# Kernel optimization log

Measured on AMD Instinct MI355X. Metric: run time of the kernel, lower is better.

The kernel has to match this reference:

```python
import jax, jax.numpy as jnp
import numpy as np

# NF4 codebook (bitsandbytes normal-float-4 quantiles)
NF4 = jnp.array([-1.0, -0.6961928009986877, -0.5250730514526367, -0.39491748809814453,
                 -0.28444138169288635, -0.18477343022823334, -0.09105003625154495, 0.0,
                 0.07958029955625534, 0.16093020141124725, 0.24611230194568634, 0.33791524171829224,
                 0.44070982933044434, 0.5626170039176941, 0.7229568362236023, 1.0], dtype=jnp.float32)

BLOCK = 64           # bitsandbytes quant blocksize
OUT, IN, R = 4096, 4096, 16
SCALING = 32.0 / 16.0  # lora_alpha / r


def setup_inputs() -> dict:
    key = jax.random.key(0)
    k1, k2, k3, k4 = jax.random.split(key, 4)
    x = jax.random.normal(k1, (4096, IN), dtype=jnp.float32)
    codes = jax.random.randint(k2, (OUT, IN), 0, 16, dtype=jnp.int32)
    scales = jax.random.uniform(k3, (OUT * IN // BLOCK,), dtype=jnp.float32) * 0.1
    lora_A = jax.random.normal(k4, (R, IN), dtype=jnp.float32) * (1.0 / np.sqrt(IN))
    lora_B = jax.random.normal(jax.random.fold_in(key, 7), (OUT, R), dtype=jnp.float32) * 0.02
    return {"x": x, "codes": codes, "scales": scales, "lora_A": lora_A, "lora_B": lora_B}


def dequantize_nf4(codes, scales):
    # codes: [OUT, IN] int in [0,16); scales: one absmax scale per BLOCK contiguous elements
    w = NF4[codes].reshape(-1, BLOCK) * scales[:, None]
    return w.reshape(OUT, IN)  # [out, in]


def reference(x, codes, scales, lora_A, lora_B):
    # Base quantized linear: dequantize then y = x @ W^T  (nn.Linear semantics)
    W = dequantize_nf4(codes, scales)               # [out, in]
    result = x @ W.T                                # [tokens, out]
    # LoRA low-rank correction (dropout p=0.0 -> identity)
    result = result + (x @ lora_A.T) @ lora_B.T * SCALING
    return result
```

## Files before the change

kernel.cpp:

```cpp
#include <hip/hip_runtime.h>
#include <hip/hip_bf16.h>

#define TOKENS 4096
#define OUTN   4096
#define INK    4096
#define RANK   16
#define KP     4160

typedef __attribute__((ext_vector_type(8))) short short8;
typedef __attribute__((ext_vector_type(4))) float f32x4;

__device__ __constant__ float NF4_TAB[16] = {
  -1.0f, -0.6961928009986877f, -0.5250730514526367f, -0.39491748809814453f,
  -0.28444138169288635f, -0.18477343022823334f, -0.09105003625154495f, 0.0f,
  0.07958029955625534f, 0.16093020141124725f, 0.24611230194568634f, 0.33791524171829224f,
  0.44070982933044434f, 0.5626170039176941f, 0.7229568362236023f, 1.0f };

__device__ __forceinline__ unsigned short f2bf(float f) {
  unsigned int u = __float_as_uint(f);
  u += 0x7FFFu + ((u >> 16) & 1u);
  return (unsigned short)(u >> 16);
}

__global__ __launch_bounds__(256) void prep_x_kernel(const float* __restrict__ x,
                                                     const float* __restrict__ loraA,
                                                     unsigned short* __restrict__ Xbf) {
  const int r0 = blockIdx.x * 4;
  const int t = threadIdx.x;
  const int lane = t & 63;
  const int wave = t >> 6;

  float xv[4][16];
  #pragma unroll
  for (int rv = 0; rv < 4; ++rv) {
    const float* xrow = x + (size_t)(r0 + rv) * INK;
    unsigned short* brow = Xbf + (size_t)(r0 + rv) * KP;
    #pragma unroll
    for (int q = 0; q < 4; ++q) {
      const int e0 = q * 1024 + t * 4;
      float4 v = *(const float4*)(xrow + e0);
      xv[rv][q * 4 + 0] = v.x; xv[rv][q * 4 + 1] = v.y;
      xv[rv][q * 4 + 2] = v.z; xv[rv][q * 4 + 3] = v.w;
      ushort4 o; o.x = f2bf(v.x); o.y = f2bf(v.y); o.z = f2bf(v.z); o.w = f2bf(v.w);
      *(ushort4*)(brow + e0) = o;
    }
  }

  float p[4][16];
  #pragma unroll
  for (int a = 0; a < 4; ++a)
    #pragma unroll
    for (int b = 0; b < 16; ++b) p[a][b] = 0.f;

  #pragma unroll
  for (int rr = 0; rr < 16; ++rr) {
    const float* arow = loraA + (size_t)rr * INK;
    float av[16];
    #pragma unroll
    for (int q = 0; q < 4; ++q) {
      float4 v = *(const float4*)(arow + q * 1024 + t * 4);
      av[q * 4 + 0] = v.x; av[q * 4 + 1] = v.y;
      av[q * 4 + 2] = v.z; av[q * 4 + 3] = v.w;
    }
    #pragma unroll
    for (int rv = 0; rv < 4; ++rv) {
      float s = 0.f;
      #pragma unroll
      for (int j = 0; j < 16; ++j) s += xv[rv][j] * av[j];
      p[rv][rr] += s;
    }
  }

  #pragma unroll
  for (int rv = 0; rv < 4; ++rv)
    #pragma unroll
    for (int rr = 0; rr < 16; ++rr) {
      float v = p[rv][rr];
      v += __shfl_xor(v, 32); v += __shfl_xor(v, 16); v += __shfl_xor(v, 8);
      v += __shfl_xor(v, 4);  v += __shfl_xor(v, 2);  v += __shfl_xor(v, 1);
      p[rv][rr] = v;
    }
  __shared__ float red[4][64];
  if (lane == 0) {
    #pragma unroll
    for (int rv = 0; rv < 4; ++rv)
      #pragma unroll
      for (int rr = 0; rr < 16; ++rr) red[wave][rv * 16 + rr] = p[rv][rr];
  }
  __syncthreads();
  if (t < 64) {
    float s = red[0][t] + red[1][t] + red[2][t] + red[3][t];
    int rv = t >> 4, rr = t & 15;
    Xbf[(size_t)(r0 + rv) * KP + INK + rr] = f2bf(s);
  }
}

__global__ __launch_bounds__(256) void prep_w_kernel(const int* __restrict__ codes,
                                                     const float* __restrict__ scales,
                                                     const float* __restrict__ loraB,
                                                     unsigned short* __restrict__ Wbf) {
  __shared__ float tab[16];
  int t = threadIdx.x;
  if (t < 16) tab[t] = NF4_TAB[t];
  __syncthreads();
  const int row = blockIdx.x;
  const int* crow = codes + (size_t)row * INK;
  const float* srow = scales + (row << 6);
  unsigned short* wrow = Wbf + (size_t)row * KP;
  #pragma unroll
  for (int q = 0; q < 4; ++q) {
    const int e0 = q * 1024 + t * 4;
    int4 c = *(const int4*)(crow + e0);
    float sc = srow[e0 >> 6];
    ushort4 o;
    o.x = f2bf(tab[c.x] * sc);
    o.y = f2bf(tab[c.y] * sc);
    o.z = f2bf(tab[c.z] * sc);
    o.w = f2bf(tab[c.w] * sc);
    *(ushort4*)(wrow + e0) = o;
  }
  if (t < RANK) {
    wrow[INK + t] = f2bf(2.0f * loraB[row * RANK + t]);
  } else if (t < 64) {
    wrow[4112 + (t - 16)] = 0;
  }
}

__global__ __launch_bounds__(256, 2) void gemm_kernel(const unsigned short* __restrict__ Xbf,
                                                      const unsigned short* __restrict__ Wbf,
                                                      float* __restrict__ out) {
  __shared__ char lds[32768];
  char* ldsA = lds;
  char* ldsB = lds + 16384;
  const int tid  = threadIdx.x;
  const int lane = tid & 63;
  const int wave = tid >> 6;
  const int wr = wave >> 1, wc = wave & 1;
  const size_t brow = (size_t)blockIdx.y * 128;
  const size_t bcol = (size_t)blockIdx.x * 128;

  f32x4 acc[4][4];
  #pragma unroll
  for (int m = 0; m < 4; ++m)
    #pragma unroll
    for (int n = 0; n < 4; ++n) acc[m][n] = (f32x4){0.f, 0.f, 0.f, 0.f};

  const char* gA[4]; const char* gB[4]; int ldst[4];
  #pragma unroll
  for (int j = 0; j < 4; ++j) {
    int c = (wave * 4 + j) * 64 + lane;
    int r = c >> 3;
    int gkc = (c & 7) ^ (r & 7);
    gA[j] = (const char*)Xbf + ((brow + r) * KP) * 2 + gkc * 16;
    gB[j] = (const char*)Wbf + ((bcol + r) * KP) * 2 + gkc * 16;
    ldst[j] = (wave * 4 + j) * 1024;
  }

  for (int kt = 0; kt < KP / 64; ++kt) {
    const int koff = kt * 128;
    #pragma unroll
    for (int j = 0; j < 4; ++j) {
      __builtin_amdgcn_global_load_lds(
          (const __attribute__((address_space(1))) void*)(gA[j] + koff),
          (__attribute__((address_space(3))) void*)(ldsA + ldst[j]), 16, 0, 0);
      __builtin_amdgcn_global_load_lds(
          (const __attribute__((address_space(1))) void*)(gB[j] + koff),
          (__attribute__((address_space(3))) void*)(ldsB + ldst[j]), 16, 0, 0);
    }
    __syncthreads();

    short8 af[4][2], bfr[4][2];
    #pragma unroll
    for (int m = 0; m < 4; ++m) {
      int r  = wr * 64 + m * 16 + (lane & 15);
      int x0 = (lane >> 4) * 16;
      int sw = (r & 7) << 4;
      af[m][0] = *(const short8*)(ldsA + r * 128 + ((x0) ^ sw));
      af[m][1] = *(const short8*)(ldsA + r * 128 + ((64 + x0) ^ sw));
    }
    #pragma unroll
    for (int n = 0; n < 4; ++n) {
      int r  = wc * 64 + n * 16 + (lane & 15);
      int x0 = (lane >> 4) * 16;
      int sw = (r & 7) << 4;
      bfr[n][0] = *(const short8*)(ldsB + r * 128 + ((x0) ^ sw));
      bfr[n][1] = *(const short8*)(ldsB + r * 128 + ((64 + x0) ^ sw));
    }
    #pragma unroll
    for (int s = 0; s < 2; ++s)
      #pragma unroll
      for (int m = 0; m < 4; ++m)
        #pragma unroll
        for (int n = 0; n < 4; ++n)
          acc[m][n] = __builtin_amdgcn_mfma_f32_16x16x32_bf16(af[m][s], bfr[n][s], acc[m][n], 0, 0, 0);
    __syncthreads();
  }

  #pragma unroll
  for (int m = 0; m < 4; ++m) {
    int row = (int)brow + wr * 64 + m * 16 + ((lane >> 4) << 2);
    #pragma unroll
    for (int n = 0; n < 4; ++n) {
      int col = (int)bcol + wc * 64 + n * 16 + (lane & 15);
      #pragma unroll
      for (int j = 0; j < 4; ++j)
        out[(size_t)(row + j) * OUTN + col] = acc[m][n][j];
    }
  }
}

extern "C" void kernel_launch(void* const* d_in, const int* in_sizes, int n_in,
                              void* d_out, int out_size, void* d_ws, size_t ws_size,
                              hipStream_t stream) {
  const float* x      = (const float*)d_in[0];
  const int*   codes  = (const int*)d_in[1];
  const float* scales = (const float*)d_in[2];
  const float* loraA  = (const float*)d_in[3];
  const float* loraB  = (const float*)d_in[4];
  float* out = (float*)d_out;

  unsigned short* Xbf = (unsigned short*)d_ws;
  unsigned short* Wbf = Xbf + (size_t)TOKENS * KP;

  prep_x_kernel<<<TOKENS / 4, 256, 0, stream>>>(x, loraA, Xbf);
  prep_w_kernel<<<OUTN, 256, 0, stream>>>(codes, scales, loraB, Wbf);

  dim3 grid(OUTN / 128, TOKENS / 128);
  gemm_kernel<<<grid, 256, 0, stream>>>(Xbf, Wbf, out);
}
```

Baseline: 325.2 us.

## Restructure GEMM into 256x256 tiles with double-buffered LDS and interleaved MFMA/load phases

The GEMM moves from 128x128 tiles with 4 waves and a single LDS buffer to 256x256 tiles with 8 waves and 128KB of dynamic LDS split into two buffers. Global-to-LDS loads for the next k-steps are issued in quarter-phases between four MFMA sub-blocks, with explicit vmcnt waits, barriers and setprio. The goal is to hide load latency behind compute and raise arithmetic intensity per byte loaded. In exchange it needs more registers and LDS, cuts occupancy, and launches only 256 blocks, which may leave some CUs idle.

```diff
diff --git a/kernel.cpp b/kernel.cpp
--- a/kernel.cpp
+++ b/kernel.cpp
@@ -6,6 +6,7 @@
 #define INK    4096
 #define RANK   16
 #define KP     4160
+#define NT     (KP/64)
 
 typedef __attribute__((ext_vector_type(8))) short short8;
 typedef __attribute__((ext_vector_type(4))) float f32x4;
@@ -126,82 +127,174 @@
   }
 }
 
-__global__ __launch_bounds__(256, 2) void gemm_kernel(const unsigned short* __restrict__ Xbf,
+#define STAGE2(BASE, OFFS, LDSB, BUF, H, KT)                                               \
+  do {                                                                                     \
+    __builtin_amdgcn_global_load_lds(                                                      \
+        (const __attribute__((address_space(1))) void*)((BASE) + (OFFS)[H][0] + (KT)*128), \
+        (__attribute__((address_space(3))) void*)((LDSB) + (BUF)*32768 + (H)*16384 + tid*16), 16, 0, 0); \
+    __builtin_amdgcn_global_load_lds(                                                      \
+        (const __attribute__((address_space(1))) void*)((BASE) + (OFFS)[H][1] + (KT)*128), \
+        (__attribute__((address_space(3))) void*)((LDSB) + (BUF)*32768 + (H)*16384 + 8192 + tid*16), 16, 0, 0); \
+  } while (0)
+
+__global__ __launch_bounds__(512, 2) void gemm_kernel(const unsigned short* __restrict__ Xbf,
                                                       const unsigned short* __restrict__ Wbf,
                                                       float* __restrict__ out) {
-  __shared__ char lds[32768];
+  extern __shared__ char lds[];
   char* ldsA = lds;
-  char* ldsB = lds + 16384;
+  char* ldsB = lds + 65536;
   const int tid  = threadIdx.x;
   const int lane = tid & 63;
   const int wave = tid >> 6;
-  const int wr = wave >> 1, wc = wave & 1;
-  const size_t brow = (size_t)blockIdx.y * 128;
-  const size_t bcol = (size_t)blockIdx.x * 128;
-
-  f32x4 acc[4][4];
-  #pragma unroll
-  for (int m = 0; m < 4; ++m)
+  const int wr = wave >> 2;
+  const int wc = wave & 3;
+  const int brow = blockIdx.y * 256;
+  const int bcol = blockIdx.x * 256;
+
+  unsigned int aoffg[2][2], boffg[2][2];
+  #pragma unroll
+  for (int h = 0; h < 2; ++h)
+    #pragma unroll
+    for (int j = 0; j < 2; ++j) {
+      int ci  = j * 512 + tid;
+      int lr  = ci >> 3;
+      int gkc = (ci & 7) ^ (lr & 7);
+      int growA = (lr & 63) | (h << 6) | ((lr >> 6) << 7);
+      int growB = (lr & 31) | (h << 5) | ((lr >> 5) << 6);
+      aoffg[h][j] = (unsigned)growA * (KP * 2) + gkc * 16;
+      boffg[h][j] = (unsigned)growB * (KP * 2) + gkc * 16;
+    }
+  const char* baseA = (const char*)Xbf + (size_t)brow * (KP * 2);
+  const char* baseB = (const char*)Wbf + (size_t)bcol * (KP * 2);
+
+  unsigned int aoff[8][2], boff[4][2];
+  #pragma unroll
+  for (int m = 0; m < 8; ++m) {
+    int R = wr * 128 + m * 16 + (lane & 15);
+    int h = (R >> 6) & 1;
+    int lr = (R & 63) | ((R >> 7) << 6);
+    #pragma unroll
+    for (int s = 0; s < 2; ++s) {
+      int c = s * 4 + (lane >> 4);
+      aoff[m][s] = h * 16384 + lr * 128 + ((c ^ (lr & 7)) * 16);
+    }
+  }
+  #pragma unroll
+  for (int n = 0; n < 4; ++n) {
+    int C = wc * 64 + n * 16 + (lane & 15);
+    int h = (C >> 5) & 1;
+    int lc = (C & 31) | ((C >> 6) << 5);
+    #pragma unroll
+    for (int s = 0; s < 2; ++s) {
+      int c = s * 4 + (lane >> 4);
+      boff[n][s] = h * 16384 + lc * 128 + ((c ^ (lc & 7)) * 16);
+    }
+  }
+
+  f32x4 acc[8][4];
+  #pragma unroll
+  for (int m = 0; m < 8; ++m)
     #pragma unroll
     for (int n = 0; n < 4; ++n) acc[m][n] = (f32x4){0.f, 0.f, 0.f, 0.f};
 
-  const char* gA[4]; const char* gB[4]; int ldst[4];
-  #pragma unroll
-  for (int j = 0; j < 4; ++j) {
-    int c = (wave * 4 + j) * 64 + lane;
-    int r = c >> 3;
-    int gkc = (c & 7) ^ (r & 7);
-    gA[j] = (const char*)Xbf + ((brow + r) * KP) * 2 + gkc * 16;
-    gB[j] = (const char*)Wbf + ((bcol + r) * KP) * 2 + gkc * 16;
-    ldst[j] = (wave * 4 + j) * 1024;
-  }
-
-  for (int kt = 0; kt < KP / 64; ++kt) {
-    const int koff = kt * 128;
-    #pragma unroll
-    for (int j = 0; j < 4; ++j) {
-      __builtin_amdgcn_global_load_lds(
-          (const __attribute__((address_space(1))) void*)(gA[j] + koff),
-          (__attribute__((address_space(3))) void*)(ldsA + ldst[j]), 16, 0, 0);
-      __builtin_amdgcn_global_load_lds(
-          (const __attribute__((address_space(1))) void*)(gB[j] + koff),
-          (__attribute__((address_space(3))) void*)(ldsB + ldst[j]), 16, 0, 0);
-    }
-    __syncthreads();
-
-    short8 af[4][2], bfr[4][2];
+  STAGE2(baseA, aoffg, ldsA, 0, 0, 0);
+  STAGE2(baseB, boffg, ldsB, 0, 0, 0);
+  STAGE2(baseA, aoffg, ldsA, 0, 1, 0);
+  STAGE2(baseB, boffg, ldsB, 0, 1, 0);
+  STAGE2(baseA, aoffg, ldsA, 1, 0, 1);
+  STAGE2(baseB, boffg, ldsB, 1, 0, 1);
+  STAGE2(baseA, aoffg, ldsA, 1, 1, 1);
+  asm volatile("s_waitcnt vmcnt(6)" ::: "memory");
+  __builtin_amdgcn_s_barrier();
+
+  short8 a_set[4][2], b0s[2][2], b1s[2][2];
+
+  for (int t = 0; t < NT; ++t) {
+    const int buf = t & 1;
+    const char* A  = ldsA + buf * 32768;
+    const char* Bb = ldsB + buf * 32768;
+
     #pragma unroll
     for (int m = 0; m < 4; ++m) {
-      int r  = wr * 64 + m * 16 + (lane & 15);
-      int x0 = (lane >> 4) * 16;
-      int sw = (r & 7) << 4;
-      af[m][0] = *(const short8*)(ldsA + r * 128 + ((x0) ^ sw));
-      af[m][1] = *(const short8*)(ldsA + r * 128 + ((64 + x0) ^ sw));
-    }
-    #pragma unroll
-    for (int n = 0; n < 4; ++n) {
-      int r  = wc * 64 + n * 16 + (lane & 15);
-      int x0 = (lane >> 4) * 16;
-      int sw = (r & 7) << 4;
-      bfr[n][0] = *(const short8*)(ldsB + r * 128 + ((x0) ^ sw));
-      bfr[n][1] = *(const short8*)(ldsB + r * 128 + ((64 + x0) ^ sw));
-    }
+      a_set[m][0] = *(const short8*)(A + aoff[m][0]);
+      a_set[m][1] = *(const short8*)(A + aoff[m][1]);
+    }
+    #pragma unroll
+    for (int n = 0; n < 2; ++n) {
+      b0s[n][0] = *(const short8*)(Bb + boff[n][0]);
+      b0s[n][1] = *(const short8*)(Bb + boff[n][1]);
+    }
+    if (t + 1 < NT) STAGE2(baseB, boffg, ldsB, (buf ^ 1), 1, t + 1);
+    __builtin_amdgcn_s_barrier();
+    __builtin_amdgcn_s_setprio(1);
     #pragma unroll
     for (int s = 0; s < 2; ++s)
       #pragma unroll
       for (int m = 0; m < 4; ++m)
         #pragma unroll
-        for (int n = 0; n < 4; ++n)
-          acc[m][n] = __builtin_amdgcn_mfma_f32_16x16x32_bf16(af[m][s], bfr[n][s], acc[m][n], 0, 0, 0);
-    __syncthreads();
-  }
-
-  #pragma unroll
-  for (int m = 0; m < 4; ++m) {
-    int row = (int)brow + wr * 64 + m * 16 + ((lane >> 4) << 2);
+        for (int n = 0; n < 2; ++n)
+          acc[m][n] = __builtin_amdgcn_mfma_f32_16x16x32_bf16(a_set[m][s], b0s[n][s], acc[m][n], 0, 0, 0);
+    __builtin_amdgcn_s_setprio(0);
+    __builtin_amdgcn_s_barrier();
+
+    #pragma unroll
+    for (int n = 0; n < 2; ++n) {
+      b1s[n][0] = *(const short8*)(Bb + boff[2 + n][0]);
+      b1s[n][1] = *(const short8*)(Bb + boff[2 + n][1]);
+    }
+    if (t + 2 < NT) STAGE2(baseA, aoffg, ldsA, buf, 0, t + 2);
+    __builtin_amdgcn_s_barrier();
+    __builtin_amdgcn_s_setprio(1);
+    #pragma unroll
+    for (int s = 0; s < 2; ++s)
+      #pragma unroll
+      for (int m = 0; m < 4; ++m)
+        #pragma unroll
+        for (int n = 0; n < 2; ++n)
+          acc[m][2 + n] = __builtin_amdgcn_mfma_f32_16x16x32_bf16(a_set[m][s], b1s[n][s], acc[m][2 + n], 0, 0, 0);
+    __builtin_amdgcn_s_setprio(0);
+    __builtin_amdgcn_s_barrier();
+
+    #pragma unroll
+    for (int m = 0; m < 4; ++m) {
+      a_set[m][0] = *(const short8*)(A + aoff[4 + m][0]);
+      a_set[m][1] = *(const short8*)(A + aoff[4 + m][1]);
+    }
+    if (t + 2 < NT) STAGE2(baseB, boffg, ldsB, buf, 0, t + 2);
+    __builtin_amdgcn_s_barrier();
+    __builtin_amdgcn_s_setprio(1);
+    #pragma unroll
+    for (int s = 0; s < 2; ++s)
+      #pragma unroll
+      for (int m = 0; m < 4; ++m)
+        #pragma unroll
+        for (int n = 0; n < 2; ++n)
+          acc[4 + m][n] = __builtin_amdgcn_mfma_f32_16x16x32_bf16(a_set[m][s], b0s[n][s], acc[4 + m][n], 0, 0, 0);
+    __builtin_amdgcn_s_setprio(0);
+    __builtin_amdgcn_s_barrier();
+
+    if (t + 2 < NT) STAGE2(baseA, aoffg, ldsA, buf, 1, t + 2);
+    if (t >= NT - 2) asm volatile("s_waitcnt vmcnt(0)" ::: "memory");
+    else             asm volatile("s_waitcnt vmcnt(6)" ::: "memory");
+    __builtin_amdgcn_s_barrier();
+    __builtin_amdgcn_s_setprio(1);
+    #pragma unroll
+    for (int s = 0; s < 2; ++s)
+      #pragma unroll
+      for (int m = 0; m < 4; ++m)
+        #pragma unroll
+        for (int n = 0; n < 2; ++n)
+          acc[4 + m][2 + n] = __builtin_amdgcn_mfma_f32_16x16x32_bf16(a_set[m][s], b1s[n][s], acc[4 + m][2 + n], 0, 0, 0);
+    __builtin_amdgcn_s_setprio(0);
+    __builtin_amdgcn_s_barrier();
+  }
+
+  #pragma unroll
+  for (int m = 0; m < 8; ++m) {
+    int row = brow + wr * 128 + m * 16 + ((lane >> 4) << 2);
     #pragma unroll
     for (int n = 0; n < 4; ++n) {
-      int col = (int)bcol + wc * 64 + n * 16 + (lane & 15);
+      int col = bcol + wc * 64 + n * 16 + (lane & 15);
       #pragma unroll
       for (int j = 0; j < 4; ++j)
         out[(size_t)(row + j) * OUTN + col] = acc[m][n][j];
@@ -225,6 +318,8 @@
   prep_x_kernel<<<TOKENS / 4, 256, 0, stream>>>(x, loraA, Xbf);
   prep_w_kernel<<<OUTN, 256, 0, stream>>>(codes, scales, loraB, Wbf);
 
-  dim3 grid(OUTN / 128, TOKENS / 128);
-  gemm_kernel<<<grid, 256, 0, stream>>>(Xbf, Wbf, out);
-}
+  static_cast<void>(hipFuncSetAttribute((const void*)gemm_kernel,
+                    hipFuncAttributeMaxDynamicSharedMemorySize, 131072));
+  dim3 grid(OUTN / 256, TOKENS / 256);
+  gemm_kernel<<<grid, 512, 131072, stream>>>(Xbf, Wbf, out);
+}
```

After: 309.0 us. 5.0% less time.
